# Kernel optimization log

Measured on AMD Instinct MI355X. Metric: run time of the kernel, lower is better.

The kernel has to match this reference:

```python
import jax, jax.numpy as jnp
import numpy as np

EPS = 1e-5

def setup_inputs() -> dict:
    key = jax.random.key(0)
    ks = jax.random.split(key, 12)
    N, d0, d1, d2, qh, qo = 8192, 128, 256, 256, 128, 1
    state = jax.random.normal(ks[0], (N, d0), dtype=jnp.float32)
    adjacent_matrix = jax.random.uniform(ks[1], (N, N), dtype=jnp.float32)
    s = 0.05
    return {
        "state": state,
        "adjacent_matrix": adjacent_matrix,
        "gamma": jnp.ones((d0,), jnp.float32),
        "beta": jnp.zeros((d0,), jnp.float32),
        "W1": jax.random.normal(ks[2], (d0, d1), jnp.float32) * s,
        "b1": jnp.zeros((d1,), jnp.float32),
        "W2": jax.random.normal(ks[3], (d1, d2), jnp.float32) * s,
        "b2": jnp.zeros((d2,), jnp.float32),
        "Wq1": jax.random.normal(ks[4], (d2, qh), jnp.float32) * s,
        "bq1": jnp.zeros((qh,), jnp.float32),
        "Wq2": jax.random.normal(ks[5], (qh, qo), jnp.float32) * s,
        "bq2": jnp.zeros((qo,), jnp.float32),
    }


def reference(state, adjacent_matrix, gamma, beta, W1, b1, W2, b2, Wq1, bq1, Wq2, bq2):
    # LinkBatchNorm: BatchNorm1d over node (batch) axis, training-mode statistics
    mean = jnp.mean(state, axis=0)
    var = jnp.var(state, axis=0)
    x = (state - mean) * jax.lax.rsqrt(var + EPS) * gamma + beta  # [N, d0]
    # GraphCNN: two layers of relu(A @ X @ W + b)
    h = jax.nn.relu(adjacent_matrix @ (x @ W1) + b1)   # [N, d1]
    h = jax.nn.relu(adjacent_matrix @ (h @ W2) + b2)   # [N, d2]
    # QNetwork: per-node MLP -> Q value
    q = jax.nn.relu(h @ Wq1 + bq1) @ Wq2 + bq2         # [N, 1]
    return q
```

## Files before the change

### kernel.cpp

```cpp
#include <hip/hip_runtime.h>
#include <stdint.h>

#define NN 8192
#define D0 128
#define D1 256
#define D2 256
#define QH 128
#define EPSV 1e-5f

using bf16x8 = __attribute__((ext_vector_type(8))) __bf16;
using f32x4  = __attribute__((ext_vector_type(4))) float;

__device__ __forceinline__ unsigned short f2bf(float f) {
    union { float f; unsigned int u; } v; v.f = f;
    unsigned int r = v.u + 0x7FFFu + ((v.u >> 16) & 1u);
    return (unsigned short)(r >> 16);
}
__device__ __forceinline__ float bf2f(unsigned short h) {
    union { unsigned int u; float f; } v; v.u = ((unsigned int)h) << 16;
    return v.f;
}
__device__ __forceinline__ unsigned pkbf(float a, float b) {
    unsigned r;
    asm("v_cvt_pk_bf16_f32 %0, %1, %2" : "=v"(r) : "v"(a), "v"(b));
    return r;
}
__device__ __forceinline__ void async_ld16(const void* g, void* l) {
    __builtin_amdgcn_global_load_lds(
        (__attribute__((address_space(1))) void*)(g),
        (__attribute__((address_space(3))) void*)(l), 16, 0, 0);
}

__global__ void k_stats(const float* __restrict__ state,
                        float* __restrict__ psum, float* __restrict__ psq,
                        float* __restrict__ acc4k, float* __restrict__ rsA) {
    int j = threadIdx.x;
    int b = blockIdx.x;
    int gid = b * 128 + j;
    if (gid < 8192) rsA[gid] = 0.f;
    if (gid < 1024) acc4k[gid] = 0.f;
    const float* p = state + (size_t)b * 32 * D0 + j;
    float s = 0.f, sq = 0.f;
#pragma unroll 4
    for (int r = 0; r < 32; ++r) { float x = p[(size_t)r * D0]; s += x; sq += x * x; }
    psum[b * D0 + j] = s;
    psq [b * D0 + j] = sq;
}

__global__ void k_finalize(const float* __restrict__ psum, const float* __restrict__ psq,
                           const float* __restrict__ gamma, const float* __restrict__ beta,
                           const float* __restrict__ W1,
                           float* __restrict__ scale, float* __restrict__ shift,
                           float* __restrict__ c1) {
    __shared__ float s_shift[D0];
    int t = threadIdx.x;
    if (t < D0) {
        float s = 0.f, sq = 0.f;
        for (int b = 0; b < 256; ++b) { s += psum[b * D0 + t]; sq += psq[b * D0 + t]; }
        float mean = s * (1.0f / NN);
        float var  = sq * (1.0f / NN) - mean * mean;
        float sc = gamma[t] * rsqrtf(var + EPSV);
        float sh = beta[t] - mean * sc;
        scale[t] = sc; shift[t] = sh; s_shift[t] = sh;
    }
    __syncthreads();
    float acc = 0.f;
    for (int k = 0; k < D0; ++k) acc += s_shift[k] * W1[(size_t)k * D1 + t];
    c1[t] = acc;
}

__global__ void k_prep_weights(const float* __restrict__ W1, const float* __restrict__ W2,
                               const float* __restrict__ scale,
                               unsigned short* __restrict__ W1st,
                               unsigned short* __restrict__ W2t) {
    int idx = blockIdx.x * 256 + threadIdx.x;
    if (idx < 32768) {
        int n = idx >> 7, k = idx & 127;
        W1st[idx] = f2bf(W1[(size_t)k * D1 + n] * scale[k]);
    } else {
        int i = idx - 32768; int n = i >> 8, k = i & 255;
        W2t[i] = f2bf(W2[(size_t)k * D2 + n]);
    }
}

template <int N, int K, bool A_FP32, bool BIAS>
__global__ __launch_bounds__(256, 4) void k_small_gemm(
        const void* __restrict__ Aptr, const unsigned short* __restrict__ Bt,
        const float* __restrict__ bias, unsigned short* __restrict__ out) {
    constexpr int WN = N / 4;
    constexpr int NJ = WN / 16;
    constexpr int BI = N / 64;
    __shared__ unsigned short Alds[32 * 32];
    __shared__ unsigned short Blds[N * 32];
    int t = threadIdx.x, lane = t & 63, w = t >> 6;
    int m0 = blockIdx.x * 32;
    int lr = lane & 15, lk = (lane >> 4) * 8;
    int wc = w * WN;
    f32x4 acc[2][NJ] = {};

    for (int kk = 0; kk < K; kk += 32) {
        __syncthreads();
        if constexpr (A_FP32) {
            const float* A = (const float*)Aptr;
            int row = t >> 3, kc = (t & 7) * 4;
            float4 v = *(const float4*)(A + (size_t)(m0 + row) * K + kk + kc);
            uint2 p;
            p.x = ((unsigned)f2bf(v.y) << 16) | f2bf(v.x);
            p.y = ((unsigned)f2bf(v.w) << 16) | f2bf(v.z);
            *(uint2*)&Alds[row * 32 + kc] = p;
        } else {
            if (w < 2) {
                const unsigned short* A = (const unsigned short*)Aptr;
                int row = w * 16 + (lane >> 2);
                async_ld16(A + (size_t)(m0 + row) * K + kk + (lane & 3) * 8, &Alds[w * 512]);
            }
        }
#pragma unroll
        for (int i = 0; i < BI; ++i) {
            int n = w * WN + i * 16 + (lane >> 2);
            async_ld16(Bt + (size_t)n * K + kk + (lane & 3) * 8, &Blds[(w * WN + i * 16) * 32]);
        }
        __syncthreads();
        bf16x8 a[2], b[NJ];
#pragma unroll
        for (int i = 0; i < 2; ++i) a[i] = *(const bf16x8*)&Alds[(i * 16 + lr) * 32 + lk];
#pragma unroll
        for (int j = 0; j < NJ; ++j) b[j] = *(const bf16x8*)&Blds[(wc + j * 16 + lr) * 32 + lk];
#pragma unroll
        for (int i = 0; i < 2; ++i)
#pragma unroll
            for (int j = 0; j < NJ; ++j)
                acc[i][j] = __builtin_amdgcn_mfma_f32_16x16x32_bf16(a[i], b[j], acc[i][j], 0, 0, 0);
    }
    int q = lane >> 4;
#pragma unroll
    for (int j = 0; j < NJ; ++j) {
        int n = wc + j * 16 + lr;
        float bv = 0.f;
        if constexpr (BIAS) bv = bias[n];
#pragma unroll
        for (int i = 0; i < 2; ++i) {
#pragma unroll
            for (int r = 0; r < 4; ++r) {
                int m = m0 + i * 16 + q * 4 + r;
                out[(size_t)m * N + n] = f2bf(acc[i][j][r] + bv);
            }
        }
    }
}

__global__ void k_transpose(const unsigned short* __restrict__ in, unsigned short* __restrict__ out,
                            float* __restrict__ colsum) {
    __shared__ unsigned short tile[64 * 68];
    __shared__ float cp[4][64];
    int t = threadIdx.x;
    int r0 = blockIdx.x * 64, c0 = blockIdx.y * 64;
#pragma unroll
    for (int p = 0; p < 4; ++p) {
        int row = (t >> 4) + p * 16, col = (t & 15) * 4;
        *(ushort4*)&tile[row * 68 + col] = *(const ushort4*)&in[(size_t)(r0 + row) * 256 + c0 + col];
    }
    __syncthreads();
    int n = t >> 2;
#pragma unroll
    for (int s = 0; s < 2; ++s) {
        int mo = (t & 3) * 16 + s * 8;
        unsigned short v[8];
#pragma unroll
        for (int e = 0; e < 8; ++e) v[e] = tile[(mo + e) * 68 + n];
        *(uint4*)&out[(size_t)(c0 + n) * NN + r0 + mo] = *(const uint4*)v;
    }
    int col = t & 63, gg = t >> 6;
    float s = 0.f;
#pragma unroll
    for (int r = 0; r < 16; ++r) s += bf2f(tile[(gg * 16 + r) * 68 + col]);
    cp[gg][col] = s;
    __syncthreads();
    if (t < 64) atomicAdd(colsum + c0 + t, cp[0][t] + cp[1][t] + cp[2][t] + cp[3][t]);
}

template <bool RSUM>
__global__ __launch_bounds__(256, 2) void k_big_gemm3(
        const float* __restrict__ A, const unsigned short* __restrict__ Yt,
        float* __restrict__ Cp, float* __restrict__ rsA) {
    __shared__ unsigned short Alds[2][128 * 32];
    __shared__ unsigned short Blds[2][256 * 32];
    int t = threadIdx.x, lane = t & 63, w = t >> 6;
    int m0 = blockIdx.x * 128;
    int kbeg = blockIdx.y * 1024;
    int wr = (w & 1) * 64, wc = (w >> 1) * 128;
    int lr = lane & 15, q = lane >> 4;
    f32x4 acc[4][8] = {};

    int arow = t >> 1;
    int axs = (arow ^ (arow >> 2)) & 3;
    int ac0 = (t & 1) * 2;
    const float* agp = A + (size_t)(m0 + arow) * NN + kbeg + (t & 1) * 16;
    int aw0 = arow * 32 + ((ac0 ^ axs) & 3) * 8;
    int aw1 = arow * 32 + (((ac0 + 1) ^ axs) & 3) * 8;

    int bxs = ((lane >> 2) ^ (lane >> 4)) & 3;
    int bchunk = (lane & 3) ^ bxs;
    const unsigned short* bgp = Yt + (size_t)(w * 64 + (lane >> 2)) * NN + kbeg + bchunk * 8;

    int xsr = (lr ^ (lr >> 2)) & 3;
    int lks = ((q ^ xsr) & 3) * 8;

    float rs = 0.f;
    float4 av0, av1, av2, av3;

    av0 = *(const float4*)(agp + 0);
    av1 = *(const float4*)(agp + 4);
    av2 = *(const float4*)(agp + 8);
    av3 = *(const float4*)(agp + 12);
#pragma unroll
    for (int c = 0; c < 4; ++c)
        async_ld16(bgp + (size_t)c * 16 * NN, &Blds[0][(w * 64 + c * 16) * 32]);
    {
        uint4 u0 = { pkbf(av0.x, av0.y), pkbf(av0.z, av0.w), pkbf(av1.x, av1.y), pkbf(av1.z, av1.w) };
        uint4 u1 = { pkbf(av2.x, av2.y), pkbf(av2.z, av2.w), pkbf(av3.x, av3.y), pkbf(av3.z, av3.w) };
        *(uint4*)&Alds[0][aw0] = u0;
        *(uint4*)&Alds[0][aw1] = u1;
    }
    if constexpr (RSUM)
        rs += av0.x + av0.y + av0.z + av0.w + av1.x + av1.y + av1.z + av1.w
            + av2.x + av2.y + av2.z + av2.w + av3.x + av3.y + av3.z + av3.w;
    __syncthreads();

#pragma unroll 2
    for (int it = 0; it < 32; ++it) {
        int p = it & 1;
        bool more = (it < 31);
        if (more) {
            int ko = (it + 1) * 32;
            av0 = *(const float4*)(agp + ko + 0);
            av1 = *(const float4*)(agp + ko + 4);
            av2 = *(const float4*)(agp + ko + 8);
            av3 = *(const float4*)(agp + ko + 12);
#pragma unroll
            for (int c = 0; c < 4; ++c)
                async_ld16(bgp + ko + (size_t)c * 16 * NN, &Blds[p ^ 1][(w * 64 + c * 16) * 32]);
        }
        bf16x8 a[4], b[8];
#pragma unroll
        for (int i = 0; i < 4; ++i) a[i] = *(const bf16x8*)&Alds[p][(wr + i * 16 + lr) * 32 + lks];
#pragma unroll
        for (int j = 0; j < 8; ++j) b[j] = *(const bf16x8*)&Blds[p][(wc + j * 16 + lr) * 32 + lks];
#pragma unroll
        for (int i = 0; i < 4; ++i)
#pragma unroll
            for (int j = 0; j < 8; ++j)
                acc[i][j] = __builtin_amdgcn_mfma_f32_16x16x32_bf16(a[i], b[j], acc[i][j], 0, 0, 0);
        if (more) {
            uint4 u0 = { pkbf(av0.x, av0.y), pkbf(av0.z, av0.w), pkbf(av1.x, av1.y), pkbf(av1.z, av1.w) };
            uint4 u1 = { pkbf(av2.x, av2.y), pkbf(av2.z, av2.w), pkbf(av3.x, av3.y), pkbf(av3.z, av3.w) };
            *(uint4*)&Alds[p ^ 1][aw0] = u0;
            *(uint4*)&Alds[p ^ 1][aw1] = u1;
            if constexpr (RSUM)
                rs += av0.x + av0.y + av0.z + av0.w + av1.x + av1.y + av1.z + av1.w
                    + av2.x + av2.y + av2.z + av2.w + av3.x + av3.y + av3.z + av3.w;
        }
        __syncthreads();
    }

    float* outp = Cp + (size_t)blockIdx.y * NN * 256;
#pragma unroll
    for (int i = 0; i < 4; ++i)
#pragma unroll
        for (int j = 0; j < 8; ++j) {
            int n = wc + j * 16 + lr;
#pragma unroll
            for (int r = 0; r < 4; ++r) {
                int m = m0 + wr + i * 16 + q * 4 + r;
                outp[(size_t)m * 256 + n] = acc[i][j][r];
            }
        }
    if constexpr (RSUM) {
        rs += __shfl_xor(rs, 1, 64);
        if ((lane & 1) == 0) atomicAdd(rsA + m0 + w * 32 + (lane >> 1), rs);
    }
}

__global__ void k_s2(const float* __restrict__ colB, const float* __restrict__ colH1,
                     const float* __restrict__ W2, float* __restrict__ s2) {
    int n = threadIdx.x;
    float acc = 0.f;
    for (int k = 0; k < 256; ++k) acc += colH1[k] * W2[(size_t)k * 256 + n];
    s2[n] = colB[n] - acc;
}

__global__ __launch_bounds__(256) void k_reduce8(
        const float* __restrict__ Cp, const float* __restrict__ rsA,
        const float* __restrict__ bias, const float* __restrict__ sn,
        unsigned short* __restrict__ out, float* __restrict__ colH1) {
    __shared__ float rs_s[16];
    __shared__ float cs[4][256];
    int t = threadIdx.x;
    int m0 = blockIdx.x * 16;
    const size_t S = (size_t)NN * 256;
    if (t < 16) rs_s[t] = rsA[m0 + t] * (1.0f / 8192.0f);
    __syncthreads();
    int g = t >> 6, cq = (t & 63) * 4;
    float4 snv = *(const float4*)(sn + cq);
    float4 bv  = *(const float4*)(bias + cq);
    float c0 = 0.f, c1a = 0.f, c2 = 0.f, c3 = 0.f;
#pragma unroll
    for (int r4 = 0; r4 < 4; ++r4) {
        int row = g * 4 + r4;
        size_t base = (size_t)(m0 + row) * 256 + cq;
        float4 a = {0.f, 0.f, 0.f, 0.f};
#pragma unroll
        for (int s = 0; s < 8; ++s) {
            float4 p = *(const float4*)(Cp + (size_t)s * S + base);
            a.x += p.x; a.y += p.y; a.z += p.z; a.w += p.w;
        }
        float rsv = rs_s[row];
        float x0 = fmaxf(a.x + bv.x - rsv * snv.x, 0.f);
        float x1 = fmaxf(a.y + bv.y - rsv * snv.y, 0.f);
        float x2 = fmaxf(a.z + bv.z - rsv * snv.z, 0.f);
        float x3 = fmaxf(a.w + bv.w - rsv * snv.w, 0.f);
        ushort4 o; o.x = f2bf(x0); o.y = f2bf(x1); o.z = f2bf(x2); o.w = f2bf(x3);
        *(ushort4*)(out + base) = o;
        c0 += x0; c1a += x1; c2 += x2; c3 += x3;
    }
    cs[g][cq] = c0; cs[g][cq + 1] = c1a; cs[g][cq + 2] = c2; cs[g][cq + 3] = c3;
    __syncthreads();
    float tot = cs[0][t] + cs[1][t] + cs[2][t] + cs[3][t];
    atomicAdd(colH1 + t, tot);
}

__global__ __launch_bounds__(256) void k_reduce_qhead(
        const float* __restrict__ Cp, const float* __restrict__ rsA,
        const float* __restrict__ bias, const float* __restrict__ sn,
        const float* __restrict__ Wq1, const float* __restrict__ bq1,
        const float* __restrict__ Wq2, const float* __restrict__ bq2,
        float* __restrict__ out) {
    __shared__ float sh[16][256];
    __shared__ float rs_s[16];
    __shared__ float red[4][8];
    int t = threadIdx.x;
    int m0 = blockIdx.x * 16;
    const size_t S = (size_t)NN * 256;
    if (t < 16) rs_s[t] = rsA[m0 + t] * (1.0f / 8192.0f);
    __syncthreads();
    int g = t >> 6, cq = (t & 63) * 4;
    float4 snv = *(const float4*)(sn + cq);
    float4 bv  = *(const float4*)(bias + cq);
#pragma unroll
    for (int r4 = 0; r4 < 4; ++r4) {
        int row = g * 4 + r4;
        size_t base = (size_t)(m0 + row) * 256 + cq;
        float4 a = {0.f, 0.f, 0.f, 0.f};
#pragma unroll
        for (int s = 0; s < 8; ++s) {
            float4 p = *(const float4*)(Cp + (size_t)s * S + base);
            a.x += p.x; a.y += p.y; a.z += p.z; a.w += p.w;
        }
        float rsv = rs_s[row];
        float4 o;
        o.x = fmaxf(a.x + bv.x - rsv * snv.x, 0.f);
        o.y = fmaxf(a.y + bv.y - rsv * snv.y, 0.f);
        o.z = fmaxf(a.z + bv.z - rsv * snv.z, 0.f);
        o.w = fmaxf(a.w + bv.w - rsv * snv.w, 0.f);
        *(float4*)&sh[row][cq] = o;
    }
    __syncthreads();
    int h = t & 127, rg = t >> 7;
    float acc[8] = {};
    const float* wq = Wq1 + h;
    for (int n4 = 0; n4 < 64; ++n4) {
        int n = n4 * 4;
        float wa = wq[(size_t)(n + 0) * QH];
        float wb = wq[(size_t)(n + 1) * QH];
        float wcc = wq[(size_t)(n + 2) * QH];
        float wd = wq[(size_t)(n + 3) * QH];
#pragma unroll
        for (int r = 0; r < 8; ++r) {
            float4 sv = *(const float4*)&sh[rg * 8 + r][n];
            acc[r] = fmaf(sv.x, wa, fmaf(sv.y, wb, fmaf(sv.z, wcc, fmaf(sv.w, wd, acc[r]))));
        }
    }
    float b1v = bq1[h], w2v = Wq2[h];
    int wid = t >> 6, lane = t & 63;
#pragma unroll
    for (int r = 0; r < 8; ++r) {
        float v = fmaxf(acc[r] + b1v, 0.f) * w2v;
#pragma unroll
        for (int d = 32; d > 0; d >>= 1) v += __shfl_down(v, d, 64);
        if (lane == 0) red[wid][r] = v;
    }
    __syncthreads();
    if (t < 16) {
        int rg2 = t >> 3, r = t & 7;
        out[m0 + rg2 * 8 + r] = red[rg2 * 2][r] + red[rg2 * 2 + 1][r] + bq2[0];
    }
}

extern "C" void kernel_launch(void* const* d_in, const int* in_sizes, int n_in,
                              void* d_out, int out_size, void* d_ws, size_t ws_size,
                              hipStream_t stream) {
    const float* state = (const float*)d_in[0];
    const float* adj   = (const float*)d_in[1];
    const float* gamma = (const float*)d_in[2];
    const float* beta  = (const float*)d_in[3];
    const float* W1    = (const float*)d_in[4];
    const float* b1    = (const float*)d_in[5];
    const float* W2    = (const float*)d_in[6];
    const float* b2    = (const float*)d_in[7];
    const float* Wq1   = (const float*)d_in[8];
    const float* bq1   = (const float*)d_in[9];
    const float* Wq2   = (const float*)d_in[10];
    const float* bq2   = (const float*)d_in[11];
    float* out = (float*)d_out;

    char* ws = (char*)d_ws;
    float* psum  = (float*)(ws + 0);
    float* psq   = (float*)(ws + 131072);
    float* scale = (float*)(ws + 262144);
    float* shift = (float*)(ws + 262656);
    float* c1    = (float*)(ws + 263168);
    float* colA  = (float*)(ws + 264192);
    float* colB  = (float*)(ws + 265216);
    float* colH1 = (float*)(ws + 266240);
    float* s2    = (float*)(ws + 267264);
    unsigned short* W1st = (unsigned short*)(ws + 268288);
    unsigned short* W2t  = (unsigned short*)(ws + 333824);
    unsigned short* Ybuf = (unsigned short*)(ws + (size_t)1  * (1u << 20));
    unsigned short* Ytb  = (unsigned short*)(ws + (size_t)5  * (1u << 20));
    unsigned short* Hbuf = (unsigned short*)(ws + (size_t)9  * (1u << 20));
    float*          rsA  = (float*)(ws + (size_t)14 * (1u << 20));
    float*          Cp   = (float*)(ws + (size_t)22 * (1u << 20));

    k_stats<<<256, 128, 0, stream>>>(state, psum, psq, colA, rsA);
    k_finalize<<<1, 256, 0, stream>>>(psum, psq, gamma, beta, W1, scale, shift, c1);
    k_prep_weights<<<384, 256, 0, stream>>>(W1, W2, scale, W1st, W2t);

    k_small_gemm<256, 128, true, true><<<256, 256, 0, stream>>>(state, W1st, c1, Ybuf);
    k_transpose<<<dim3(128, 4), 256, 0, stream>>>(Ybuf, Ytb, colA);
    k_big_gemm3<true><<<dim3(64, 8), 256, 0, stream>>>(adj, Ytb, Cp, rsA);
    k_reduce8<<<512, 256, 0, stream>>>(Cp, rsA, b1, colA, Hbuf, colH1);

    k_small_gemm<256, 256, false, false><<<256, 256, 0, stream>>>(Hbuf, W2t, nullptr, Ybuf);
    k_transpose<<<dim3(128, 4), 256, 0, stream>>>(Ybuf, Ytb, colB);
    k_s2<<<1, 256, 0, stream>>>(colB, colH1, W2, s2);
    k_big_gemm3<false><<<dim3(64, 8), 256, 0, stream>>>(adj, Ytb, Cp, rsA);
    k_reduce_qhead<<<512, 256, 0, stream>>>(Cp, rsA, b2, s2, Wq1, bq1, Wq2, bq2, out);
}
```

Measured before the change: 644.7 us.

## Split big GEMM across 8 waves with smaller per-wave tiles

The main adjacency GEMM now runs with 512 threads (8 waves) per block instead of 256. Each wave computes a 64x64 output tile instead of 64x128, which halves its accumulator registers. Global-to-LDS load duties are redistributed so each thread converts one 8-float A segment and issues two async B loads. The row-sum reduction gains an extra shuffle step. The aim is more resident waves and better latency hiding on the memory-bound fp32 A stream, at the cost of less register-level reuse of the A fragments per wave.

```diff
diff --git a/kernel.cpp b/kernel.cpp
--- a/kernel.cpp
+++ b/kernel.cpp
@@ -180,7 +180,7 @@
 }
 
 template <bool RSUM>
-__global__ __launch_bounds__(256, 2) void k_big_gemm3(
+__global__ __launch_bounds__(512, 4) void k_big_gemm4(
         const float* __restrict__ A, const unsigned short* __restrict__ Yt,
         float* __restrict__ Cp, float* __restrict__ rsA) {
     __shared__ unsigned short Alds[2][128 * 32];
@@ -188,43 +188,36 @@
     int t = threadIdx.x, lane = t & 63, w = t >> 6;
     int m0 = blockIdx.x * 128;
     int kbeg = blockIdx.y * 1024;
-    int wr = (w & 1) * 64, wc = (w >> 1) * 128;
+    int wr = (w & 1) * 64, wc = (w >> 1) * 64;
     int lr = lane & 15, q = lane >> 4;
-    f32x4 acc[4][8] = {};
-
-    int arow = t >> 1;
+    f32x4 acc[4][4] = {};
+
+    int arow = t >> 2, aseg = t & 3;
     int axs = (arow ^ (arow >> 2)) & 3;
-    int ac0 = (t & 1) * 2;
-    const float* agp = A + (size_t)(m0 + arow) * NN + kbeg + (t & 1) * 16;
-    int aw0 = arow * 32 + ((ac0 ^ axs) & 3) * 8;
-    int aw1 = arow * 32 + (((ac0 + 1) ^ axs) & 3) * 8;
-
-    int bxs = ((lane >> 2) ^ (lane >> 4)) & 3;
-    int bchunk = (lane & 3) ^ bxs;
-    const unsigned short* bgp = Yt + (size_t)(w * 64 + (lane >> 2)) * NN + kbeg + bchunk * 8;
+    const float* agp = A + (size_t)(m0 + arow) * NN + kbeg + aseg * 8;
+    int awr = arow * 32 + ((aseg ^ axs) & 3) * 8;
+
+    int srow = lane >> 2;
+    int hsw = (lane & 3) ^ ((srow ^ (srow >> 2)) & 3);
+    const unsigned short* bg0 = Yt + (size_t)(w * 32 + srow) * NN + kbeg + hsw * 8;
+    const unsigned short* bg1 = Yt + (size_t)(w * 32 + 16 + srow) * NN + kbeg + hsw * 8;
 
     int xsr = (lr ^ (lr >> 2)) & 3;
     int lks = ((q ^ xsr) & 3) * 8;
 
     float rs = 0.f;
-    float4 av0, av1, av2, av3;
+    float4 av0, av1;
 
     av0 = *(const float4*)(agp + 0);
     av1 = *(const float4*)(agp + 4);
-    av2 = *(const float4*)(agp + 8);
-    av3 = *(const float4*)(agp + 12);
-#pragma unroll
-    for (int c = 0; c < 4; ++c)
-        async_ld16(bgp + (size_t)c * 16 * NN, &Blds[0][(w * 64 + c * 16) * 32]);
+    async_ld16(bg0, &Blds[0][w * 1024]);
+    async_ld16(bg1, &Blds[0][w * 1024 + 512]);
     {
-        uint4 u0 = { pkbf(av0.x, av0.y), pkbf(av0.z, av0.w), pkbf(av1.x, av1.y), pkbf(av1.z, av1.w) };
-        uint4 u1 = { pkbf(av2.x, av2.y), pkbf(av2.z, av2.w), pkbf(av3.x, av3.y), pkbf(av3.z, av3.w) };
-        *(uint4*)&Alds[0][aw0] = u0;
-        *(uint4*)&Alds[0][aw1] = u1;
+        uint4 u = { pkbf(av0.x, av0.y), pkbf(av0.z, av0.w), pkbf(av1.x, av1.y), pkbf(av1.z, av1.w) };
+        *(uint4*)&Alds[0][awr] = u;
     }
     if constexpr (RSUM)
-        rs += av0.x + av0.y + av0.z + av0.w + av1.x + av1.y + av1.z + av1.w
-            + av2.x + av2.y + av2.z + av2.w + av3.x + av3.y + av3.z + av3.w;
+        rs += av0.x + av0.y + av0.z + av0.w + av1.x + av1.y + av1.z + av1.w;
     __syncthreads();
 
 #pragma unroll 2
@@ -233,32 +226,26 @@
         bool more = (it < 31);
         if (more) {
             int ko = (it + 1) * 32;
-            av0 = *(const float4*)(agp + ko + 0);
+            av0 = *(const float4*)(agp + ko);
             av1 = *(const float4*)(agp + ko + 4);
-            av2 = *(const float4*)(agp + ko + 8);
-            av3 = *(const float4*)(agp + ko + 12);
-#pragma unroll
-            for (int c = 0; c < 4; ++c)
-                async_ld16(bgp + ko + (size_t)c * 16 * NN, &Blds[p ^ 1][(w * 64 + c * 16) * 32]);
-        }
-        bf16x8 a[4], b[8];
+            async_ld16(bg0 + ko, &Blds[p ^ 1][w * 1024]);
+            async_ld16(bg1 + ko, &Blds[p ^ 1][w * 1024 + 512]);
+        }
+        bf16x8 a[4];
 #pragma unroll
         for (int i = 0; i < 4; ++i) a[i] = *(const bf16x8*)&Alds[p][(wr + i * 16 + lr) * 32 + lks];
 #pragma unroll
-        for (int j = 0; j < 8; ++j) b[j] = *(const bf16x8*)&Blds[p][(wc + j * 16 + lr) * 32 + lks];
-#pragma unroll
-        for (int i = 0; i < 4; ++i)
-#pragma unroll
-            for (int j = 0; j < 8; ++j)
-                acc[i][j] = __builtin_amdgcn_mfma_f32_16x16x32_bf16(a[i], b[j], acc[i][j], 0, 0, 0);
+        for (int j = 0; j < 4; ++j) {
+            bf16x8 b = *(const bf16x8*)&Blds[p][(wc + j * 16 + lr) * 32 + lks];
+#pragma unroll
+            for (int i = 0; i < 4; ++i)
+                acc[i][j] = __builtin_amdgcn_mfma_f32_16x16x32_bf16(a[i], b, acc[i][j], 0, 0, 0);
+        }
         if (more) {
-            uint4 u0 = { pkbf(av0.x, av0.y), pkbf(av0.z, av0.w), pkbf(av1.x, av1.y), pkbf(av1.z, av1.w) };
-            uint4 u1 = { pkbf(av2.x, av2.y), pkbf(av2.z, av2.w), pkbf(av3.x, av3.y), pkbf(av3.z, av3.w) };
-            *(uint4*)&Alds[p ^ 1][aw0] = u0;
-            *(uint4*)&Alds[p ^ 1][aw1] = u1;
+            uint4 u = { pkbf(av0.x, av0.y), pkbf(av0.z, av0.w), pkbf(av1.x, av1.y), pkbf(av1.z, av1.w) };
+            *(uint4*)&Alds[p ^ 1][awr] = u;
             if constexpr (RSUM)
-                rs += av0.x + av0.y + av0.z + av0.w + av1.x + av1.y + av1.z + av1.w
-                    + av2.x + av2.y + av2.z + av2.w + av3.x + av3.y + av3.z + av3.w;
+                rs += av0.x + av0.y + av0.z + av0.w + av1.x + av1.y + av1.z + av1.w;
         }
         __syncthreads();
     }
@@ -267,7 +254,7 @@
 #pragma unroll
     for (int i = 0; i < 4; ++i)
 #pragma unroll
-        for (int j = 0; j < 8; ++j) {
+        for (int j = 0; j < 4; ++j) {
             int n = wc + j * 16 + lr;
 #pragma unroll
             for (int r = 0; r < 4; ++r) {
@@ -277,7 +264,8 @@
         }
     if constexpr (RSUM) {
         rs += __shfl_xor(rs, 1, 64);
-        if ((lane & 1) == 0) atomicAdd(rsA + m0 + w * 32 + (lane >> 1), rs);
+        rs += __shfl_xor(rs, 2, 64);
+        if ((lane & 3) == 0) atomicAdd(rsA + m0 + arow, rs);
     }
 }
 
@@ -437,12 +425,12 @@
 
     k_small_gemm<256, 128, true, true><<<256, 256, 0, stream>>>(state, W1st, c1, Ybuf);
     k_transpose<<<dim3(128, 4), 256, 0, stream>>>(Ybuf, Ytb, colA);
-    k_big_gemm3<true><<<dim3(64, 8), 256, 0, stream>>>(adj, Ytb, Cp, rsA);
+    k_big_gemm4<true><<<dim3(64, 8), 512, 0, stream>>>(adj, Ytb, Cp, rsA);
     k_reduce8<<<512, 256, 0, stream>>>(Cp, rsA, b1, colA, Hbuf, colH1);
 
     k_small_gemm<256, 256, false, false><<<256, 256, 0, stream>>>(Hbuf, W2t, nullptr, Ybuf);
     k_transpose<<<dim3(128, 4), 256, 0, stream>>>(Ybuf, Ytb, colB);
     k_s2<<<1, 256, 0, stream>>>(colB, colH1, W2, s2);
-    k_big_gemm3<false><<<dim3(64, 8), 256, 0, stream>>>(adj, Ytb, Cp, rsA);
+    k_big_gemm4<false><<<dim3(64, 8), 512, 0, stream>>>(adj, Ytb, Cp, rsA);
     k_reduce_qhead<<<512, 256, 0, stream>>>(Cp, rsA, b2, s2, Wq1, bq1, Wq2, bq2, out);
 }
```

New measurement: 638.6 us. No clear change (-0.9%).
